# Performance work log

Measured on AMD Instinct MI355X. Metric: run time of the kernel, lower is better.

## Reference

```python
import jax, jax.numpy as jnp
import numpy as np

NEG = -1e30  # log-space 'zero' (bf16/fp32 safe, avoids -inf NaN propagation)
EPS = 1e-7   # keras.backend.epsilon(), added before log as in ctc_batch_cost


def _lse3(a, b, c):
    # stable logsumexp over three stacked log-values
    m = jnp.maximum(jnp.maximum(a, b), c)
    return m + jnp.log(jnp.exp(a - m) + jnp.exp(b - m) + jnp.exp(c - m))


def setup_inputs() -> dict:
    key = jax.random.key(0)
    k1, k2 = jax.random.split(key)
    B, T, C, L = 256, 512, 1024, 64
    # y_pred must be softmax probabilities (ctc_batch_cost takes log(p + eps))
    y_pred = jax.nn.softmax(jax.random.normal(k1, (B, T, C), dtype=jnp.float32), axis=-1)
    # labels in [0, C-1): never equal to blank (= C-1); no -1 padding here,
    # so label_length = L for every row, matching the layer's mask computation
    y_true = jax.random.randint(k2, (B, L), 0, C - 1).astype(jnp.int32)
    return {"y_true": y_true, "y_pred": y_pred}


def reference(y_true, y_pred):
    B, T, C = y_pred.shape
    L = y_true.shape[1]
    blank = C - 1  # tf classic CTC: blank is the last class
    S = 2 * L + 1

    lp = jnp.log(y_pred + EPS)                      # [B, T, C]
    ll = jnp.sum(y_true != -1, axis=1)              # [B] label lengths (mask of -1)

    # extended label sequence: blank, l1, blank, l2, ..., blank
    labels = jnp.where(y_true < 0, blank, y_true)
    ext = jnp.full((B, S), blank, dtype=y_true.dtype).at[:, 1::2].set(labels)

    # emission log-probs gathered at extended-label classes: e[b,t,s] = lp[b,t,ext[b,s]]
    idx = jnp.broadcast_to(ext[:, None, :], (B, T, S))
    e = jnp.take_along_axis(lp, idx, axis=2)        # [B, T, S]

    pos = jnp.arange(S)
    valid = pos[None, :] < (2 * ll + 1)[:, None]    # states within this row's DP band
    # skip transition s-2 -> s allowed iff ext[s] != blank and ext[s] != ext[s-2]
    allow2 = jnp.zeros((B, S), bool).at[:, 2:].set(
        (ext[:, 2:] != blank) & (ext[:, 2:] != ext[:, :-2]))

    alpha0 = jnp.where((pos[None, :] < 2) & valid, e[:, 0, :], NEG)  # [B, S]
    neg_col = jnp.full((B, 1), NEG, dtype=lp.dtype)

    def step(alpha, e_t):
        p1 = jnp.concatenate([neg_col, alpha[:, :-1]], axis=1)
        p2 = jnp.concatenate([neg_col, neg_col, alpha[:, :-2]], axis=1)
        p2 = jnp.where(allow2, p2, NEG)
        new = jnp.where(valid, e_t + _lse3(alpha, p1, p2), NEG)
        return new, None

    # input_length = T for every row (as computed in the layer)
    alpha_T, _ = jax.lax.scan(step, alpha0, jnp.swapaxes(e, 0, 1)[1:])

    a_last = jnp.take_along_axis(alpha_T, (2 * ll)[:, None], axis=1)[:, 0]
    a_prev = jnp.take_along_axis(alpha_T, jnp.maximum(2 * ll - 1, 0)[:, None], axis=1)[:, 0]
    a_prev = jnp.where(ll > 0, a_prev, NEG)
    loss = -jnp.logaddexp(a_last, a_prev)           # [B]
    return loss[:, None]                            # ctc_batch_cost returns [B, 1]
```

## Files before the change

### kernel.cpp

```cpp
#include <hip/hip_runtime.h>


constexpr int B = 256, T = 512, C = 1024, L = 64;
constexpr int BLK   = 1024;
constexpr int NW    = BLK / 64;
constexpr int CHUNK = 128;
constexpr int TPW   = CHUNK / NW;
constexpr int STRIDE = 66;
#define EPSV (1e-7f)
constexpr float LN2F = 0.69314718055994530942f;

__device__ __forceinline__ float flog2(float x) { return __builtin_amdgcn_logf(x); }

__global__ __launch_bounds__(BLK, 1)
void ctc_loss_kernel(const int* __restrict__ y_true,
                     const float* __restrict__ y_pred,
                     float* __restrict__ out) {
    __shared__ float e_lds[CHUNK * STRIDE];

    const int b    = blockIdx.x;
    const int tid  = threadIdx.x;
    const int lane = tid & 63;
    const int wave = tid >> 6;
    const float* p = y_pred + (size_t)b * T * C;

    int lab = y_true[b * L + lane];
    int cls = (lab < 0) ? (C - 1) : lab;
    unsigned long long msk = __ballot(lab != -1);
    int ll = __popcll(msk);
    int clsprev = __shfl_up(cls, 1);
    const bool allow = (lane > 0) && (cls != C - 1) && (cls != clsprev);

    float bv = 0.f, lv = 0.f, b64 = 0.f;
    float shift = 0.f;

    for (int c = 0; c < T / CHUNK; ++c) {
        const int tbase = c * CHUNK;

        {
            const int t0 = tbase + wave * TPW;
            float r[TPW];
#pragma unroll
            for (int k = 0; k < TPW; ++k)
                r[k] = p[(size_t)(t0 + k) * C + cls];
            float vb = 0.f;
            if (lane < TPW)
                vb = p[(size_t)(t0 + lane) * C + (C - 1)];
#pragma unroll
            for (int k = 0; k < TPW; ++k)
                e_lds[(t0 - tbase + k) * STRIDE + lane] = r[k] + EPSV;
            if (lane < TPW)
                e_lds[(t0 - tbase + lane) * STRIDE + 64] = vb + EPSV;
        }
        __syncthreads();

        if (wave == 0) {
            for (int g = 0; g < CHUNK; g += 8) {
                float elr[8], ebr[8];
#pragma unroll
                for (int k = 0; k < 8; ++k) {
                    elr[k] = e_lds[(g + k) * STRIDE + lane];
                    ebr[k] = e_lds[(g + k) * STRIDE + 64];
                }
#pragma unroll
                for (int k = 0; k < 8; ++k) {
                    const int t = tbase + g + k;
                    const float el = elr[k], eb = ebr[k];
                    if (t == 0) {
                        bv  = (lane == 0) ? eb : 0.f;
                        lv  = (lane == 0 && ll >= 1) ? el : 0.f;
                        b64 = 0.f;
                    } else {
                        float lprev = __shfl_up(lv, 1);
                        if (lane == 0) lprev = 0.f;
                        float nb   = (bv + lprev) * eb;
                        float p2   = allow ? lprev : 0.f;
                        float nl   = (lv + bv + p2) * el;
                        float nb64 = (b64 + lv) * eb;
                        bv = nb; lv = nl; b64 = nb64;
                    }
                    if ((t & 7) == 7) {
                        float mx = fmaxf(fmaxf(bv, lv), b64);
#pragma unroll
                        for (int s = 1; s < 64; s <<= 1)
                            mx = fmaxf(mx, __shfl_xor(mx, s));
                        unsigned u = __float_as_uint(mx);
                        int e = (int)((u >> 23) & 0xFF);
                        int sb = 314 - e;
                        if (sb > 254) sb = 254;
                        if (sb < 1)   sb = 1;
                        float scale = __uint_as_float((unsigned)sb << 23);
                        bv *= scale; lv *= scale; b64 *= scale;
                        shift += (float)(sb - 127);
                    }
                }
            }
        }
        __syncthreads();
    }

    if (wave == 0) {
        float a_last = (ll == 64) ? __shfl(b64, 63) : __shfl(bv, ll);
        float a_prev = (ll > 0)   ? __shfl(lv, ll - 1) : 0.f;
        if (lane == 0) {
            float s = a_last + a_prev;
            out[b] = -(flog2(s) - shift) * LN2F;
        }
    }
}

extern "C" void kernel_launch(void* const* d_in, const int* in_sizes, int n_in,
                              void* d_out, int out_size, void* d_ws, size_t ws_size,
                              hipStream_t stream) {
    const int*   y_true = (const int*)d_in[0];
    const float* y_pred = (const float*)d_in[1];
    float*       out    = (float*)d_out;
    ctc_loss_kernel<<<B, BLK, 0, stream>>>(y_true, y_pred, out);
}
```

Before: 676.3 us.

## Double-buffer emission tiles, use producer waves, and unroll the CTC recurrence two steps

```diff
diff --git a/kernel.cpp b/kernel.cpp
--- a/kernel.cpp
+++ b/kernel.cpp
@@ -2,21 +2,35 @@
 
 
 constexpr int B = 256, T = 512, C = 1024, L = 64;
-constexpr int BLK   = 1024;
-constexpr int NW    = BLK / 64;
-constexpr int CHUNK = 128;
-constexpr int TPW   = CHUNK / NW;
+constexpr int BLK    = 1024;
+constexpr int NW     = BLK / 64;
+constexpr int CHUNK  = 128;
+constexpr int NCH    = T / CHUNK;
 constexpr int STRIDE = 66;
 #define EPSV (1e-7f)
 constexpr float LN2F = 0.69314718055994530942f;
 
 __device__ __forceinline__ float flog2(float x) { return __builtin_amdgcn_logf(x); }
 
+__device__ __forceinline__ float wave_max_f32(float m) {
+#define DPP_MAX(ctrl)                                                        \
+    m = fmaxf(m, __int_as_float(__builtin_amdgcn_update_dpp(                 \
+            __float_as_int(m), __float_as_int(m), (ctrl), 0xf, 0xf, false)));
+    DPP_MAX(0x111);
+    DPP_MAX(0x112);
+    DPP_MAX(0x114);
+    DPP_MAX(0x118);
+    DPP_MAX(0x142);
+    DPP_MAX(0x143);
+#undef DPP_MAX
+    return __int_as_float(__builtin_amdgcn_readlane(__float_as_int(m), 63));
+}
+
 __global__ __launch_bounds__(BLK, 1)
 void ctc_loss_kernel(const int* __restrict__ y_true,
                      const float* __restrict__ y_pred,
                      float* __restrict__ out) {
-    __shared__ float e_lds[CHUNK * STRIDE];
+    __shared__ float e_lds[2][CHUNK * STRIDE];
 
     const int b    = blockIdx.x;
     const int tid  = threadIdx.x;
@@ -30,69 +44,112 @@
     int ll = __popcll(msk);
     int clsprev = __shfl_up(cls, 1);
     const bool allow = (lane > 0) && (cls != C - 1) && (cls != clsprev);
+    int am1i = __shfl_up((int)allow, 1);
+    const bool am1 = (lane > 0) && (am1i != 0);
 
-    float bv = 0.f, lv = 0.f, b64 = 0.f;
-    float shift = 0.f;
+    {
+        const int r0 = wave * (CHUNK / NW);
+        float rv[CHUNK / NW];
+#pragma unroll
+        for (int k = 0; k < CHUNK / NW; ++k)
+            rv[k] = p[(size_t)(r0 + k) * C + cls];
+        float vb = 0.f;
+        if (lane < CHUNK / NW)
+            vb = p[(size_t)(r0 + lane) * C + (C - 1)];
+#pragma unroll
+        for (int k = 0; k < CHUNK / NW; ++k)
+            e_lds[0][(r0 + k) * STRIDE + lane] = rv[k] + EPSV;
+        if (lane < CHUNK / NW)
+            e_lds[0][(r0 + lane) * STRIDE + 64] = vb + EPSV;
+    }
+    __syncthreads();
 
-    for (int c = 0; c < T / CHUNK; ++c) {
-        const int tbase = c * CHUNK;
+    float bst = 0.f, lst = 0.f, b64 = 0.f;
+    int shift = 0;
 
-        {
-            const int t0 = tbase + wave * TPW;
-            float r[TPW];
+    for (int c = 0; c < NCH; ++c) {
+        if (wave != 0) {
+            if (c + 1 < NCH) {
+                float* dst = e_lds[(c + 1) & 1];
+                const int tb = (c + 1) * CHUNK;
+                float rv[9];
 #pragma unroll
-            for (int k = 0; k < TPW; ++k)
-                r[k] = p[(size_t)(t0 + k) * C + cls];
-            float vb = 0.f;
-            if (lane < TPW)
-                vb = p[(size_t)(t0 + lane) * C + (C - 1)];
+                for (int k = 0; k < 9; ++k) {
+                    int r = (wave - 1) + 15 * k;
+                    rv[k] = (r < CHUNK) ? p[(size_t)(tb + r) * C + cls] : 0.f;
+                }
+                float vb = 0.f;
+                int rbk = (wave - 1) + 15 * lane;
+                if (lane < 9 && rbk < CHUNK)
+                    vb = p[(size_t)(tb + rbk) * C + (C - 1)];
 #pragma unroll
-            for (int k = 0; k < TPW; ++k)
-                e_lds[(t0 - tbase + k) * STRIDE + lane] = r[k] + EPSV;
-            if (lane < TPW)
-                e_lds[(t0 - tbase + lane) * STRIDE + 64] = vb + EPSV;
-        }
-        __syncthreads();
-
-        if (wave == 0) {
+                for (int k = 0; k < 9; ++k) {
+                    int r = (wave - 1) + 15 * k;
+                    if (r < CHUNK) dst[r * STRIDE + lane] = rv[k] + EPSV;
+                }
+                if (lane < 9 && rbk < CHUNK)
+                    dst[rbk * STRIDE + 64] = vb + EPSV;
+            }
+        } else {
+            const float* tile = e_lds[c & 1];
             for (int g = 0; g < CHUNK; g += 8) {
-                float elr[8], ebr[8];
+                float elr[8], ebr[8], elm1[4];
 #pragma unroll
                 for (int k = 0; k < 8; ++k) {
-                    elr[k] = e_lds[(g + k) * STRIDE + lane];
-                    ebr[k] = e_lds[(g + k) * STRIDE + 64];
+                    elr[k] = tile[(g + k) * STRIDE + lane];
+                    ebr[k] = tile[(g + k) * STRIDE + 64];
                 }
 #pragma unroll
-                for (int k = 0; k < 8; ++k) {
-                    const int t = tbase + g + k;
-                    const float el = elr[k], eb = ebr[k];
-                    if (t == 0) {
-                        bv  = (lane == 0) ? eb : 0.f;
-                        lv  = (lane == 0 && ll >= 1) ? el : 0.f;
-                        b64 = 0.f;
-                    } else {
-                        float lprev = __shfl_up(lv, 1);
-                        if (lane == 0) lprev = 0.f;
-                        float nb   = (bv + lprev) * eb;
-                        float p2   = allow ? lprev : 0.f;
-                        float nl   = (lv + bv + p2) * el;
-                        float nb64 = (b64 + lv) * eb;
-                        bv = nb; lv = nl; b64 = nb64;
+                for (int j = 0; j < 4; ++j)
+                    elm1[j] = (lane == 0) ? 0.f
+                                          : tile[(g + 2 * j) * STRIDE + (lane - 1)];
+
+#define PAIRSTEP(K) {                                                   \
+    float sl  = __shfl_up(lst, 1);                                      \
+    float sbv = __shfl_up(bst, 1);                                      \
+    float s2l = __shfl_up(lst, 2);                                      \
+    if (lane == 0) { sl = 0.f; sbv = 0.f; }                             \
+    if (lane < 2)  s2l = 0.f;                                           \
+    float b1  = (bst + sl) * ebr[K];                                    \
+    float l1  = (lst + bst + (allow ? sl : 0.f)) * elr[K];              \
+    float t64 = (b64 + lst) * ebr[K];                                   \
+    float sl1 = (lane == 0) ? 0.f                                       \
+              : ((sl + sbv + (am1 ? s2l : 0.f)) * elm1[(K) / 2]);       \
+    bst = (b1 + sl1) * ebr[(K) + 1];                                    \
+    lst = (l1 + b1 + (allow ? sl1 : 0.f)) * elr[(K) + 1];               \
+    b64 = (t64 + l1) * ebr[(K) + 1]; }
+
+                if (c == 0 && g == 0) {
+                    bst = (lane == 0) ? ebr[0] : 0.f;
+                    lst = (lane == 0 && ll >= 1) ? elr[0] : 0.f;
+                    b64 = 0.f;
+                    {
+                        float sl = __shfl_up(lst, 1);
+                        if (lane == 0) sl = 0.f;
+                        float nb  = (bst + sl) * ebr[1];
+                        float nl  = (lst + bst + (allow ? sl : 0.f)) * elr[1];
+                        float n64 = (b64 + lst) * ebr[1];
+                        bst = nb; lst = nl; b64 = n64;
                     }
-                    if ((t & 7) == 7) {
-                        float mx = fmaxf(fmaxf(bv, lv), b64);
-#pragma unroll
-                        for (int s = 1; s < 64; s <<= 1)
-                            mx = fmaxf(mx, __shfl_xor(mx, s));
-                        unsigned u = __float_as_uint(mx);
-                        int e = (int)((u >> 23) & 0xFF);
-                        int sb = 314 - e;
-                        if (sb > 254) sb = 254;
-                        if (sb < 1)   sb = 1;
-                        float scale = __uint_as_float((unsigned)sb << 23);
-                        bv *= scale; lv *= scale; b64 *= scale;
-                        shift += (float)(sb - 127);
-                    }
+                    PAIRSTEP(2)
+                    PAIRSTEP(4)
+                    PAIRSTEP(6)
+                } else {
+                    PAIRSTEP(0)
+                    PAIRSTEP(2)
+                    PAIRSTEP(4)
+                    PAIRSTEP(6)
+                }
+#undef PAIRSTEP
+                {
+                    float m = wave_max_f32(fmaxf(fmaxf(bst, lst), b64));
+                    unsigned u = __float_as_uint(m);
+                    int e = (int)((u >> 23) & 0xFF);
+                    int sb = 314 - e;
+                    sb = sb > 254 ? 254 : (sb < 1 ? 1 : sb);
+                    float sc = __uint_as_float((unsigned)sb << 23);
+                    bst *= sc; lst *= sc; b64 *= sc;
+                    shift += sb - 127;
                 }
             }
         }
@@ -100,11 +157,11 @@
     }
 
     if (wave == 0) {
-        float a_last = (ll == 64) ? __shfl(b64, 63) : __shfl(bv, ll);
-        float a_prev = (ll > 0)   ? __shfl(lv, ll - 1) : 0.f;
+        float a_last = (ll == 64) ? __shfl(b64, 63) : __shfl(bst, ll);
+        float a_prev = (ll > 0)   ? __shfl(lst, ll - 1) : 0.f;
         if (lane == 0) {
             float s = a_last + a_prev;
-            out[b] = -(flog2(s) - shift) * LN2F;
+            out[b] = -(flog2(s) - (float)shift) * LN2F;
         }
     }
 }
```

New measurement: 669.3 us. About the same (-1.0%).
